# Optimization experiments

Measured on AMD Instinct MI355X. Metric: run time of the kernel, lower is better.

## Reference

```python
import jax, jax.numpy as jnp
import numpy as np

N = 500_000      # active input voxels
C = 64           # feature channels
B = 2            # batch size
RES = 256        # input spatial resolution (coords in [0, RES))
FACTOR = 2       # downsample factor (init kwarg)


def setup_inputs() -> dict:
    key = jax.random.key(0)
    k1, k2, k3 = jax.random.split(key, 3)
    feats = jax.random.normal(k1, (N, C), dtype=jnp.float32)
    bidx = jax.random.randint(k2, (N, 1), 0, B, dtype=jnp.int32)
    xyz = jax.random.randint(k3, (N, 3), 0, RES, dtype=jnp.int32)
    coords = jnp.concatenate([bidx, xyz], axis=1)  # [N, 4] = (b, x, y, z)
    return {"feats": feats, "coords": coords}


def reference(feats, coords):
    """Sparse voxel downsample: coord hashing + dedup + scatter-mean pooling.

    Returns (new_feats [N, C], new_coords [N, 4]); rows beyond the number of
    unique downsampled voxels are zero-feature / coord = -1 padding (JAX needs
    static shapes; torch original returns only the n_unique valid rows).
    """
    res = RES // FACTOR  # static spatial extent after downsampling
    b = coords[:, 0].astype(jnp.int32)
    xyz = coords[:, 1:] // FACTOR  # [N, 3]
    # linear hash code = ((b*res + x)*res + y)*res + z
    code = ((b * res + xyz[:, 0]) * res + xyz[:, 1]) * res + xyz[:, 2]
    uniq, inv = jnp.unique(code, size=N, fill_value=-1, return_inverse=True)
    # mean pooling with include_self=False == segment_sum / segment_count
    counts = jax.ops.segment_sum(jnp.ones((N,), feats.dtype), inv, num_segments=N)
    sums = jax.ops.segment_sum(feats, inv, num_segments=N)  # [N, C]
    new_feats = sums / jnp.maximum(counts, 1.0)[:, None]
    # decode unique codes back to (b, x, y, z)
    valid = counts > 0
    z = uniq % res
    y = (uniq // res) % res
    x = (uniq // (res * res)) % res
    nb = uniq // (res * res * res)
    new_coords = jnp.stack([nb, x, y, z], axis=-1).astype(jnp.int32)
    new_coords = jnp.where(valid[:, None], new_coords, -1)
    return new_feats, new_coords
```

## Files before the change

### kernel.cpp

```cpp
#include <hip/hip_runtime.h>


#define RES2 128
#define NCODES (2 * 128 * 128 * 128)
#define NW (NCODES / 4)
#define HBLK 4096

__global__ void count_codes(const int* __restrict__ coords,
                            unsigned* __restrict__ cnt8,
                            int* __restrict__ codes, int n) {
    int i = blockIdx.x * 256 + threadIdx.x;
    if (i >= n) return;
    const int4 v = reinterpret_cast<const int4*>(coords)[i];
    int code = (((v.x * RES2 + (v.y >> 1)) * RES2 + (v.z >> 1)) * RES2) + (v.w >> 1);
    codes[i] = code;
    atomicAdd(&cnt8[code >> 2], 1u << (8 * (code & 3)));
}

__global__ void block_flag_sum(const unsigned* __restrict__ cnt8,
                               unsigned* __restrict__ btot) {
    __shared__ unsigned sh[256];
    int t = threadIdx.x;
    unsigned w = cnt8[blockIdx.x * 256 + t];
    unsigned s = ((w & 0xFFu) != 0) + ((w & 0xFF00u) != 0) +
                 ((w & 0xFF0000u) != 0) + ((w & 0xFF000000u) != 0);
    sh[t] = s;
    __syncthreads();
    for (int off = 128; off > 0; off >>= 1) {
        if (t < off) sh[t] += sh[t + off];
        __syncthreads();
    }
    if (t == 0) btot[blockIdx.x] = sh[0];
}

__global__ void scan_block_totals(unsigned* __restrict__ btot,
                                  unsigned* __restrict__ nuq) {
    __shared__ unsigned sh[1024];
    int t = threadIdx.x;
    int base = t * 4;
    unsigned v[4], e[4], s = 0;
#pragma unroll
    for (int j = 0; j < 4; ++j) { v[j] = btot[base + j]; e[j] = s; s += v[j]; }
    sh[t] = s;
    __syncthreads();
    for (int off = 1; off < 1024; off <<= 1) {
        unsigned add = (t >= off) ? sh[t - off] : 0u;
        __syncthreads();
        sh[t] += add;
        __syncthreads();
    }
    unsigned excl = (t == 0) ? 0u : sh[t - 1];
#pragma unroll
    for (int j = 0; j < 4; ++j) btot[base + j] = excl + e[j];
    if (t == 1023) *nuq = sh[1023];
}

__global__ void scan_write(const unsigned* __restrict__ cnt8,
                           const unsigned* __restrict__ btot,
                           unsigned* __restrict__ rank_tab,
                           float* __restrict__ outF,
                           float* __restrict__ outC) {
    __shared__ unsigned sh[256];
    int t = threadIdx.x;
    unsigned w = cnt8[blockIdx.x * 256 + t];
    unsigned c4[4] = {w & 0xFFu, (w >> 8) & 0xFFu, (w >> 16) & 0xFFu, w >> 24};
    unsigned e[4], s = 0;
#pragma unroll
    for (int j = 0; j < 4; ++j) { e[j] = s; s += (c4[j] != 0); }
    sh[t] = s;
    __syncthreads();
    for (int off = 1; off < 256; off <<= 1) {
        unsigned add = (t >= off) ? sh[t - off] : 0u;
        __syncthreads();
        sh[t] += add;
        __syncthreads();
    }
    unsigned texcl = ((t == 0) ? 0u : sh[t - 1]) + btot[blockIdx.x];
    int cbase = (blockIdx.x * 256 + t) * 4;
#pragma unroll
    for (int j = 0; j < 4; ++j) {
        if (c4[j]) {
            unsigned r = texcl + e[j];
            int code = cbase + j;
            rank_tab[code] = r | (c4[j] << 19);
            int z = code & 127;
            int y = (code >> 7) & 127;
            int x = (code >> 14) & 127;
            int b = code >> 21;
            reinterpret_cast<float4*>(outC)[r] =
                make_float4((float)b, (float)x, (float)y, (float)z);
            if (c4[j] >= 2) {
                float4* row = reinterpret_cast<float4*>(outF + (size_t)r * 64);
                const float4 zz = make_float4(0.f, 0.f, 0.f, 0.f);
#pragma unroll
                for (int q = 0; q < 16; ++q) row[q] = zz;
            }
        }
    }
}

__global__ void tail_pad(const unsigned* __restrict__ nuq,
                         float* __restrict__ outF,
                         float* __restrict__ outC, int n) {
    int r = blockIdx.x * 256 + threadIdx.x;
    if (r >= n || r < (int)*nuq) return;
    float4* row = reinterpret_cast<float4*>(outF + (size_t)r * 64);
    const float4 zz = make_float4(0.f, 0.f, 0.f, 0.f);
#pragma unroll
    for (int q = 0; q < 16; ++q) row[q] = zz;
    reinterpret_cast<float4*>(outC)[r] = make_float4(-1.f, -1.f, -1.f, -1.f);
}

__global__ void scatter8(const float4* __restrict__ feats4,
                         const int* __restrict__ codes,
                         const unsigned* __restrict__ rank_tab,
                         float4* __restrict__ outF4, int n) {
    int tid = blockIdx.x * 256 + threadIdx.x;
    int lane = threadIdx.x & 63;
    int wave = tid >> 6;
    int q = lane >> 4;
    int sub = lane & 15;
    int ib = wave * 8;
    int i0 = ib + q;
    int i1 = ib + 4 + q;
    if (ib + 7 < n) {
        int c0 = codes[i0];
        int c1 = codes[i1];
        unsigned p0 = rank_tab[c0];
        unsigned p1 = rank_tab[c1];
        float4 v0 = feats4[(size_t)i0 * 16 + sub];
        float4 v1 = feats4[(size_t)i1 * 16 + sub];
        unsigned r0 = p0 & 0x7FFFFu, u0 = p0 >> 19;
        unsigned r1 = p1 & 0x7FFFFu, u1 = p1 >> 19;
        if (u0 == 1) {
            outF4[(size_t)r0 * 16 + sub] = v0;
        } else {
            float s = 1.0f / (float)u0;
            float* d = (float*)(outF4 + (size_t)r0 * 16 + sub);
            atomicAdd(d + 0, v0.x * s); atomicAdd(d + 1, v0.y * s);
            atomicAdd(d + 2, v0.z * s); atomicAdd(d + 3, v0.w * s);
        }
        if (u1 == 1) {
            outF4[(size_t)r1 * 16 + sub] = v1;
        } else {
            float s = 1.0f / (float)u1;
            float* d = (float*)(outF4 + (size_t)r1 * 16 + sub);
            atomicAdd(d + 0, v1.x * s); atomicAdd(d + 1, v1.y * s);
            atomicAdd(d + 2, v1.z * s); atomicAdd(d + 3, v1.w * s);
        }
    } else {
        for (int h = 0; h < 2; ++h) {
            int i = ib + h * 4 + q;
            if (i >= n) continue;
            int c = codes[i];
            unsigned p = rank_tab[c];
            unsigned r = p & 0x7FFFFu, u = p >> 19;
            float4 v = feats4[(size_t)i * 16 + sub];
            if (u == 1) {
                outF4[(size_t)r * 16 + sub] = v;
            } else {
                float s = 1.0f / (float)u;
                float* d = (float*)(outF4 + (size_t)r * 16 + sub);
                atomicAdd(d + 0, v.x * s); atomicAdd(d + 1, v.y * s);
                atomicAdd(d + 2, v.z * s); atomicAdd(d + 3, v.w * s);
            }
        }
    }
}

extern "C" void kernel_launch(void* const* d_in, const int* in_sizes, int n_in,
                              void* d_out, int out_size, void* d_ws, size_t ws_size,
                              hipStream_t stream) {
    const float* feats = (const float*)d_in[0];
    const int* coords = (const int*)d_in[1];
    const int n = in_sizes[1] / 4;

    float* outF = (float*)d_out;
    float* outC = outF + (size_t)n * 64;

    unsigned* cnt8 = (unsigned*)d_ws;
    unsigned* btot = cnt8 + NW;
    unsigned* nuq = btot + HBLK;
    int* codes = (int*)(nuq + 1);
    unsigned* rank_tab = (unsigned*)(codes + n);

    hipMemsetAsync(cnt8, 0, (size_t)NW * sizeof(unsigned), stream);

    count_codes<<<(n + 255) / 256, 256, 0, stream>>>(coords, cnt8, codes, n);
    block_flag_sum<<<HBLK, 256, 0, stream>>>(cnt8, btot);
    scan_block_totals<<<1, 1024, 0, stream>>>(btot, nuq);
    scan_write<<<HBLK, 256, 0, stream>>>(cnt8, btot, rank_tab, outF, outC);
    tail_pad<<<(n + 255) / 256, 256, 0, stream>>>(nuq, outF, outC, n);

    int waves = (n + 7) / 8;
    int blocks = (waves * 64 + 255) / 256;
    scatter8<<<blocks, 256, 0, stream>>>((const float4*)feats, codes,
                                         rank_tab, (float4*)outF, n);
}
```

Baseline: 133.7 us.

## Replace atomic scatter-mean with counting-sort bucketing and per-row gather

Extends the scan to carry both unique-count and member-count prefix sums in one 64-bit value, so each unique voxel gets a contiguous bucket. A new fill_sorted pass places input indices into these buckets with an atomic counter per row. A gather kernel then averages each bucket's features in registers and writes every output row exactly once, padding rows included. This removes the float atomics, the row pre-zeroing and the separate tail-pad kernel, at the cost of an extra index pass, extra workspace, 64-bit scans, and random feature gathers with variable per-row loop lengths.

```diff
diff --git a/kernel.cpp b/kernel.cpp
--- a/kernel.cpp
+++ b/kernel.cpp
@@ -5,6 +5,8 @@
 #define NCODES (2 * 128 * 128 * 128)
 #define NW (NCODES / 4)
 #define HBLK 4096
+
+typedef unsigned long long u64;
 
 __global__ void count_codes(const int* __restrict__ coords,
                             unsigned* __restrict__ cnt8,
@@ -17,13 +19,15 @@
     atomicAdd(&cnt8[code >> 2], 1u << (8 * (code & 3)));
 }
 
-__global__ void block_flag_sum(const unsigned* __restrict__ cnt8,
-                               unsigned* __restrict__ btot) {
-    __shared__ unsigned sh[256];
+__global__ void block_sums(const unsigned* __restrict__ cnt8,
+                           u64* __restrict__ btot) {
+    __shared__ u64 sh[256];
     int t = threadIdx.x;
     unsigned w = cnt8[blockIdx.x * 256 + t];
-    unsigned s = ((w & 0xFFu) != 0) + ((w & 0xFF00u) != 0) +
-                 ((w & 0xFF0000u) != 0) + ((w & 0xFF000000u) != 0);
+    unsigned c0 = w & 0xFFu, c1 = (w >> 8) & 0xFFu,
+             c2 = (w >> 16) & 0xFFu, c3 = w >> 24;
+    u64 s = ((u64)(c0 + c1 + c2 + c3) << 32) |
+            (u64)((c0 != 0) + (c1 != 0) + (c2 != 0) + (c3 != 0));
     sh[t] = s;
     __syncthreads();
     for (int off = 128; off > 0; off >>= 1) {
@@ -33,136 +37,163 @@
     if (t == 0) btot[blockIdx.x] = sh[0];
 }
 
-__global__ void scan_block_totals(unsigned* __restrict__ btot,
-                                  unsigned* __restrict__ nuq) {
-    __shared__ unsigned sh[1024];
+__global__ void scan_totals(u64* __restrict__ btot, unsigned* __restrict__ nuq) {
+    __shared__ u64 sh[1024];
     int t = threadIdx.x;
     int base = t * 4;
-    unsigned v[4], e[4], s = 0;
+    u64 v[4], e[4], s = 0;
 #pragma unroll
     for (int j = 0; j < 4; ++j) { v[j] = btot[base + j]; e[j] = s; s += v[j]; }
     sh[t] = s;
     __syncthreads();
     for (int off = 1; off < 1024; off <<= 1) {
-        unsigned add = (t >= off) ? sh[t - off] : 0u;
+        u64 add = (t >= off) ? sh[t - off] : 0ull;
         __syncthreads();
         sh[t] += add;
         __syncthreads();
     }
-    unsigned excl = (t == 0) ? 0u : sh[t - 1];
+    u64 excl = (t == 0) ? 0ull : sh[t - 1];
 #pragma unroll
     for (int j = 0; j < 4; ++j) btot[base + j] = excl + e[j];
-    if (t == 1023) *nuq = sh[1023];
+    if (t == 1023) *nuq = (unsigned)(sh[1023] & 0xFFFFFFFFull);
 }
 
 __global__ void scan_write(const unsigned* __restrict__ cnt8,
-                           const unsigned* __restrict__ btot,
+                           const u64* __restrict__ btot,
                            unsigned* __restrict__ rank_tab,
-                           float* __restrict__ outF,
-                           float* __restrict__ outC) {
-    __shared__ unsigned sh[256];
+                           unsigned* __restrict__ uniq_cc,
+                           unsigned* __restrict__ row_end) {
+    __shared__ u64 sh[256];
     int t = threadIdx.x;
     unsigned w = cnt8[blockIdx.x * 256 + t];
     unsigned c4[4] = {w & 0xFFu, (w >> 8) & 0xFFu, (w >> 16) & 0xFFu, w >> 24};
-    unsigned e[4], s = 0;
-#pragma unroll
-    for (int j = 0; j < 4; ++j) { e[j] = s; s += (c4[j] != 0); }
+    u64 e[4], s = 0;
+#pragma unroll
+    for (int j = 0; j < 4; ++j) {
+        e[j] = s;
+        s += ((u64)c4[j] << 32) | (u64)(c4[j] != 0);
+    }
     sh[t] = s;
     __syncthreads();
     for (int off = 1; off < 256; off <<= 1) {
-        unsigned add = (t >= off) ? sh[t - off] : 0u;
+        u64 add = (t >= off) ? sh[t - off] : 0ull;
         __syncthreads();
         sh[t] += add;
         __syncthreads();
     }
-    unsigned texcl = ((t == 0) ? 0u : sh[t - 1]) + btot[blockIdx.x];
+    u64 texcl = ((t == 0) ? 0ull : sh[t - 1]) + btot[blockIdx.x];
     int cbase = (blockIdx.x * 256 + t) * 4;
 #pragma unroll
     for (int j = 0; j < 4; ++j) {
         if (c4[j]) {
-            unsigned r = texcl + e[j];
+            unsigned r = (unsigned)((texcl + e[j]) & 0xFFFFFFFFull);
+            unsigned st = (unsigned)((texcl + e[j]) >> 32);
             int code = cbase + j;
-            rank_tab[code] = r | (c4[j] << 19);
-            int z = code & 127;
-            int y = (code >> 7) & 127;
-            int x = (code >> 14) & 127;
-            int b = code >> 21;
-            reinterpret_cast<float4*>(outC)[r] =
-                make_float4((float)b, (float)x, (float)y, (float)z);
-            if (c4[j] >= 2) {
-                float4* row = reinterpret_cast<float4*>(outF + (size_t)r * 64);
-                const float4 zz = make_float4(0.f, 0.f, 0.f, 0.f);
-#pragma unroll
-                for (int q = 0; q < 16; ++q) row[q] = zz;
-            }
-        }
-    }
-}
-
-__global__ void tail_pad(const unsigned* __restrict__ nuq,
-                         float* __restrict__ outF,
-                         float* __restrict__ outC, int n) {
-    int r = blockIdx.x * 256 + threadIdx.x;
-    if (r >= n || r < (int)*nuq) return;
-    float4* row = reinterpret_cast<float4*>(outF + (size_t)r * 64);
-    const float4 zz = make_float4(0.f, 0.f, 0.f, 0.f);
-#pragma unroll
-    for (int q = 0; q < 16; ++q) row[q] = zz;
-    reinterpret_cast<float4*>(outC)[r] = make_float4(-1.f, -1.f, -1.f, -1.f);
-}
-
-__global__ void scatter8(const float4* __restrict__ feats4,
-                         const int* __restrict__ codes,
-                         const unsigned* __restrict__ rank_tab,
-                         float4* __restrict__ outF4, int n) {
+            rank_tab[code] = r;
+            uniq_cc[r] = (unsigned)code | (c4[j] << 22);
+            row_end[r] = st;
+        }
+    }
+}
+
+__global__ void fill_sorted(const int* __restrict__ codes,
+                            const unsigned* __restrict__ rank_tab,
+                            unsigned* __restrict__ row_end,
+                            int* __restrict__ sorted_idx, int n) {
+    int i = blockIdx.x * 256 + threadIdx.x;
+    if (i >= n) return;
+    unsigned r = rank_tab[codes[i]];
+    unsigned pos = atomicAdd(&row_end[r], 1u);
+    sorted_idx[pos] = i;
+}
+
+__global__ void gather16(const float4* __restrict__ feats4,
+                         const int* __restrict__ sorted_idx,
+                         const unsigned* __restrict__ row_end,
+                         const unsigned* __restrict__ uniq_cc,
+                         const unsigned* __restrict__ nuq_p,
+                         float4* __restrict__ outF4,
+                         float4* __restrict__ outC4, int n) {
     int tid = blockIdx.x * 256 + threadIdx.x;
+    int wave = tid >> 6;
     int lane = threadIdx.x & 63;
-    int wave = tid >> 6;
     int q = lane >> 4;
     int sub = lane & 15;
-    int ib = wave * 8;
-    int i0 = ib + q;
-    int i1 = ib + 4 + q;
-    if (ib + 7 < n) {
-        int c0 = codes[i0];
-        int c1 = codes[i1];
-        unsigned p0 = rank_tab[c0];
-        unsigned p1 = rank_tab[c1];
-        float4 v0 = feats4[(size_t)i0 * 16 + sub];
-        float4 v1 = feats4[(size_t)i1 * 16 + sub];
-        unsigned r0 = p0 & 0x7FFFFu, u0 = p0 >> 19;
-        unsigned r1 = p1 & 0x7FFFFu, u1 = p1 >> 19;
-        if (u0 == 1) {
-            outF4[(size_t)r0 * 16 + sub] = v0;
-        } else {
-            float s = 1.0f / (float)u0;
-            float* d = (float*)(outF4 + (size_t)r0 * 16 + sub);
-            atomicAdd(d + 0, v0.x * s); atomicAdd(d + 1, v0.y * s);
-            atomicAdd(d + 2, v0.z * s); atomicAdd(d + 3, v0.w * s);
-        }
-        if (u1 == 1) {
-            outF4[(size_t)r1 * 16 + sub] = v1;
-        } else {
-            float s = 1.0f / (float)u1;
-            float* d = (float*)(outF4 + (size_t)r1 * 16 + sub);
-            atomicAdd(d + 0, v1.x * s); atomicAdd(d + 1, v1.y * s);
-            atomicAdd(d + 2, v1.z * s); atomicAdd(d + 3, v1.w * s);
+    int rb = wave * 16 + q;
+    int nuq = (int)*nuq_p;
+
+    int r[4];
+    bool ok[4];
+#pragma unroll
+    for (int k = 0; k < 4; ++k) { r[k] = rb + k * 4; ok[k] = (r[k] < nuq); }
+
+    bool allv = (wave * 16 + 15 < n) & ok[0] & ok[1] & ok[2] & ok[3];
+    if (allv) {
+        unsigned en[4], cc[4];
+#pragma unroll
+        for (int k = 0; k < 4; ++k) en[k] = row_end[r[k]];
+#pragma unroll
+        for (int k = 0; k < 4; ++k) cc[k] = uniq_cc[r[k]];
+        int cnt[4], st[4], i0[4];
+#pragma unroll
+        for (int k = 0; k < 4; ++k) {
+            cnt[k] = (int)(cc[k] >> 22);
+            st[k] = (int)en[k] - cnt[k];
+        }
+#pragma unroll
+        for (int k = 0; k < 4; ++k) i0[k] = sorted_idx[st[k]];
+        float4 a[4];
+#pragma unroll
+        for (int k = 0; k < 4; ++k) a[k] = feats4[(size_t)i0[k] * 16 + sub];
+#pragma unroll
+        for (int k = 0; k < 4; ++k) {
+            if (cnt[k] > 1) {
+                for (int m = 1; m < cnt[k]; ++m) {
+                    int i = sorted_idx[st[k] + m];
+                    float4 v = feats4[(size_t)i * 16 + sub];
+                    a[k].x += v.x; a[k].y += v.y; a[k].z += v.z; a[k].w += v.w;
+                }
+                float sc = 1.0f / (float)cnt[k];
+                a[k].x *= sc; a[k].y *= sc; a[k].z *= sc; a[k].w *= sc;
+            }
+            outF4[(size_t)r[k] * 16 + sub] = a[k];
+            if (sub == 0) {
+                unsigned code = cc[k] & 0x3FFFFFu;
+                outC4[r[k]] = make_float4((float)(code >> 21),
+                                          (float)((code >> 14) & 127),
+                                          (float)((code >> 7) & 127),
+                                          (float)(code & 127));
+            }
         }
     } else {
-        for (int h = 0; h < 2; ++h) {
-            int i = ib + h * 4 + q;
-            if (i >= n) continue;
-            int c = codes[i];
-            unsigned p = rank_tab[c];
-            unsigned r = p & 0x7FFFFu, u = p >> 19;
-            float4 v = feats4[(size_t)i * 16 + sub];
-            if (u == 1) {
-                outF4[(size_t)r * 16 + sub] = v;
+#pragma unroll
+        for (int k = 0; k < 4; ++k) {
+            if (r[k] >= n) continue;
+            if (ok[k]) {
+                unsigned en = row_end[r[k]];
+                unsigned cc = uniq_cc[r[k]];
+                int cnt = (int)(cc >> 22);
+                int st = (int)en - cnt;
+                float4 a = make_float4(0.f, 0.f, 0.f, 0.f);
+                for (int m = 0; m < cnt; ++m) {
+                    int i = sorted_idx[st + m];
+                    float4 v = feats4[(size_t)i * 16 + sub];
+                    a.x += v.x; a.y += v.y; a.z += v.z; a.w += v.w;
+                }
+                float sc = 1.0f / (float)cnt;
+                a.x *= sc; a.y *= sc; a.z *= sc; a.w *= sc;
+                outF4[(size_t)r[k] * 16 + sub] = a;
+                if (sub == 0) {
+                    unsigned code = cc & 0x3FFFFFu;
+                    outC4[r[k]] = make_float4((float)(code >> 21),
+                                              (float)((code >> 14) & 127),
+                                              (float)((code >> 7) & 127),
+                                              (float)(code & 127));
+                }
             } else {
-                float s = 1.0f / (float)u;
-                float* d = (float*)(outF4 + (size_t)r * 16 + sub);
-                atomicAdd(d + 0, v.x * s); atomicAdd(d + 1, v.y * s);
-                atomicAdd(d + 2, v.z * s); atomicAdd(d + 3, v.w * s);
+                outF4[(size_t)r[k] * 16 + sub] = make_float4(0.f, 0.f, 0.f, 0.f);
+                if (sub == 0)
+                    outC4[r[k]] = make_float4(-1.f, -1.f, -1.f, -1.f);
             }
         }
     }
@@ -176,24 +207,28 @@
     const int n = in_sizes[1] / 4;
 
     float* outF = (float*)d_out;
-    float* outC = outF + (size_t)n * 64;
+    float4* outC4 = (float4*)(outF + (size_t)n * 64);
 
     unsigned* cnt8 = (unsigned*)d_ws;
-    unsigned* btot = cnt8 + NW;
-    unsigned* nuq = btot + HBLK;
-    int* codes = (int*)(nuq + 1);
+    u64* btot = (u64*)(cnt8 + NW);
+    unsigned* nuq = (unsigned*)(btot + HBLK);
+    int* codes = (int*)(nuq + 2);
     unsigned* rank_tab = (unsigned*)(codes + n);
+    unsigned* uniq_cc = rank_tab + NCODES;
+    unsigned* row_end = uniq_cc + n;
+    int* sorted_idx = (int*)(row_end + n);
 
     hipMemsetAsync(cnt8, 0, (size_t)NW * sizeof(unsigned), stream);
 
     count_codes<<<(n + 255) / 256, 256, 0, stream>>>(coords, cnt8, codes, n);
-    block_flag_sum<<<HBLK, 256, 0, stream>>>(cnt8, btot);
-    scan_block_totals<<<1, 1024, 0, stream>>>(btot, nuq);
-    scan_write<<<HBLK, 256, 0, stream>>>(cnt8, btot, rank_tab, outF, outC);
-    tail_pad<<<(n + 255) / 256, 256, 0, stream>>>(nuq, outF, outC, n);
-
-    int waves = (n + 7) / 8;
+    block_sums<<<HBLK, 256, 0, stream>>>(cnt8, btot);
+    scan_totals<<<1, 1024, 0, stream>>>(btot, nuq);
+    scan_write<<<HBLK, 256, 0, stream>>>(cnt8, btot, rank_tab, uniq_cc, row_end);
+    fill_sorted<<<(n + 255) / 256, 256, 0, stream>>>(codes, rank_tab, row_end, sorted_idx, n);
+
+    int waves = (n + 15) / 16;
     int blocks = (waves * 64 + 255) / 256;
-    scatter8<<<blocks, 256, 0, stream>>>((const float4*)feats, codes,
-                                         rank_tab, (float4*)outF, n);
-}
+    gather16<<<blocks, 256, 0, stream>>>((const float4*)feats, sorted_idx,
+                                         row_end, uniq_cc, nuq,
+                                         (float4*)outF, outC4, n);
+}
```

Result: faster. 125.6 us (-6.0%).

## Replace per-code rank table with per-word prefix and recompute rank in scatter

Applied to the files above, without the earlier changes.

scan_write now stores one exclusive prefix per packed count word instead of scattering a rank/count entry into a code-indexed table. scatter8 reads the count word and word prefix and recomputes the rank and multiplicity from the byte flags. This swaps scattered rank-table writes for a dense, coalesced prefix array. Singleton rows are now written with nontemporal stores. The cost is one extra dependent gather per point in scatter.

```diff
diff --git a/kernel.cpp b/kernel.cpp
--- a/kernel.cpp
+++ b/kernel.cpp
@@ -5,6 +5,8 @@
 #define NCODES (2 * 128 * 128 * 128)
 #define NW (NCODES / 4)
 #define HBLK 4096
+
+typedef float f4 __attribute__((ext_vector_type(4)));
 
 __global__ void count_codes(const int* __restrict__ coords,
                             unsigned* __restrict__ cnt8,
@@ -22,9 +24,8 @@
     __shared__ unsigned sh[256];
     int t = threadIdx.x;
     unsigned w = cnt8[blockIdx.x * 256 + t];
-    unsigned s = ((w & 0xFFu) != 0) + ((w & 0xFF00u) != 0) +
-                 ((w & 0xFF0000u) != 0) + ((w & 0xFF000000u) != 0);
-    sh[t] = s;
+    sh[t] = ((w & 0xFFu) != 0) + (((w >> 8) & 0xFFu) != 0) +
+            (((w >> 16) & 0xFFu) != 0) + ((w >> 24) != 0);
     __syncthreads();
     for (int off = 128; off > 0; off >>= 1) {
         if (t < off) sh[t] += sh[t + off];
@@ -33,8 +34,8 @@
     if (t == 0) btot[blockIdx.x] = sh[0];
 }
 
-__global__ void scan_block_totals(unsigned* __restrict__ btot,
-                                  unsigned* __restrict__ nuq) {
+__global__ void scan_totals(unsigned* __restrict__ btot,
+                            unsigned* __restrict__ nuq) {
     __shared__ unsigned sh[1024];
     int t = threadIdx.x;
     int base = t * 4;
@@ -57,12 +58,13 @@
 
 __global__ void scan_write(const unsigned* __restrict__ cnt8,
                            const unsigned* __restrict__ btot,
-                           unsigned* __restrict__ rank_tab,
-                           float* __restrict__ outF,
-                           float* __restrict__ outC) {
+                           unsigned* __restrict__ wprefix,
+                           f4* __restrict__ outF4,
+                           f4* __restrict__ outC4) {
     __shared__ unsigned sh[256];
     int t = threadIdx.x;
-    unsigned w = cnt8[blockIdx.x * 256 + t];
+    int widx = blockIdx.x * 256 + t;
+    unsigned w = cnt8[widx];
     unsigned c4[4] = {w & 0xFFu, (w >> 8) & 0xFFu, (w >> 16) & 0xFFu, w >> 24};
     unsigned e[4], s = 0;
 #pragma unroll
@@ -76,22 +78,19 @@
         __syncthreads();
     }
     unsigned texcl = ((t == 0) ? 0u : sh[t - 1]) + btot[blockIdx.x];
-    int cbase = (blockIdx.x * 256 + t) * 4;
+    wprefix[widx] = texcl;
+    int cbase = widx * 4;
 #pragma unroll
     for (int j = 0; j < 4; ++j) {
         if (c4[j]) {
             unsigned r = texcl + e[j];
             int code = cbase + j;
-            rank_tab[code] = r | (c4[j] << 19);
-            int z = code & 127;
-            int y = (code >> 7) & 127;
-            int x = (code >> 14) & 127;
-            int b = code >> 21;
-            reinterpret_cast<float4*>(outC)[r] =
-                make_float4((float)b, (float)x, (float)y, (float)z);
+            f4 cv = {(float)(code >> 21), (float)((code >> 14) & 127),
+                     (float)((code >> 7) & 127), (float)(code & 127)};
+            outC4[r] = cv;
             if (c4[j] >= 2) {
-                float4* row = reinterpret_cast<float4*>(outF + (size_t)r * 64);
-                const float4 zz = make_float4(0.f, 0.f, 0.f, 0.f);
+                f4* row = outF4 + (size_t)r * 16;
+                const f4 zz = {0.f, 0.f, 0.f, 0.f};
 #pragma unroll
                 for (int q = 0; q < 16; ++q) row[q] = zz;
             }
@@ -100,70 +99,55 @@
 }
 
 __global__ void tail_pad(const unsigned* __restrict__ nuq,
-                         float* __restrict__ outF,
-                         float* __restrict__ outC, int n) {
+                         f4* __restrict__ outF4,
+                         f4* __restrict__ outC4, int n) {
     int r = blockIdx.x * 256 + threadIdx.x;
     if (r >= n || r < (int)*nuq) return;
-    float4* row = reinterpret_cast<float4*>(outF + (size_t)r * 64);
-    const float4 zz = make_float4(0.f, 0.f, 0.f, 0.f);
+    f4* row = outF4 + (size_t)r * 16;
+    const f4 zz = {0.f, 0.f, 0.f, 0.f};
 #pragma unroll
     for (int q = 0; q < 16; ++q) row[q] = zz;
-    reinterpret_cast<float4*>(outC)[r] = make_float4(-1.f, -1.f, -1.f, -1.f);
+    f4 mm = {-1.f, -1.f, -1.f, -1.f};
+    outC4[r] = mm;
 }
 
-__global__ void scatter8(const float4* __restrict__ feats4,
+__global__ void scatter8(const f4* __restrict__ feats4,
                          const int* __restrict__ codes,
-                         const unsigned* __restrict__ rank_tab,
-                         float4* __restrict__ outF4, int n) {
+                         const unsigned* __restrict__ cnt8,
+                         const unsigned* __restrict__ wprefix,
+                         f4* __restrict__ outF4, int n) {
     int tid = blockIdx.x * 256 + threadIdx.x;
     int lane = threadIdx.x & 63;
     int wave = tid >> 6;
     int q = lane >> 4;
     int sub = lane & 15;
     int ib = wave * 8;
-    int i0 = ib + q;
-    int i1 = ib + 4 + q;
-    if (ib + 7 < n) {
-        int c0 = codes[i0];
-        int c1 = codes[i1];
-        unsigned p0 = rank_tab[c0];
-        unsigned p1 = rank_tab[c1];
-        float4 v0 = feats4[(size_t)i0 * 16 + sub];
-        float4 v1 = feats4[(size_t)i1 * 16 + sub];
-        unsigned r0 = p0 & 0x7FFFFu, u0 = p0 >> 19;
-        unsigned r1 = p1 & 0x7FFFFu, u1 = p1 >> 19;
-        if (u0 == 1) {
-            outF4[(size_t)r0 * 16 + sub] = v0;
+
+#pragma unroll
+    for (int h = 0; h < 2; ++h) {
+        int i = ib + h * 4 + q;
+        if (i >= n) continue;
+        int c = codes[i];
+        unsigned w = cnt8[c >> 2];
+        unsigned base = wprefix[c >> 2];
+        int j = c & 3;
+        unsigned cnt = (w >> (8 * j)) & 0xFFu;
+        unsigned occ = 0;
+        if (j > 0) occ += ((w & 0xFFu) != 0);
+        if (j > 1) occ += (((w >> 8) & 0xFFu) != 0);
+        if (j > 2) occ += (((w >> 16) & 0xFFu) != 0);
+        unsigned r = base + occ;
+        f4 v = feats4[(size_t)i * 16 + sub];
+        f4* dst = outF4 + (size_t)r * 16 + sub;
+        if (cnt == 1) {
+            __builtin_nontemporal_store(v, dst);
         } else {
-            float s = 1.0f / (float)u0;
-            float* d = (float*)(outF4 + (size_t)r0 * 16 + sub);
-            atomicAdd(d + 0, v0.x * s); atomicAdd(d + 1, v0.y * s);
-            atomicAdd(d + 2, v0.z * s); atomicAdd(d + 3, v0.w * s);
-        }
-        if (u1 == 1) {
-            outF4[(size_t)r1 * 16 + sub] = v1;
-        } else {
-            float s = 1.0f / (float)u1;
-            float* d = (float*)(outF4 + (size_t)r1 * 16 + sub);
-            atomicAdd(d + 0, v1.x * s); atomicAdd(d + 1, v1.y * s);
-            atomicAdd(d + 2, v1.z * s); atomicAdd(d + 3, v1.w * s);
-        }
-    } else {
-        for (int h = 0; h < 2; ++h) {
-            int i = ib + h * 4 + q;
-            if (i >= n) continue;
-            int c = codes[i];
-            unsigned p = rank_tab[c];
-            unsigned r = p & 0x7FFFFu, u = p >> 19;
-            float4 v = feats4[(size_t)i * 16 + sub];
-            if (u == 1) {
-                outF4[(size_t)r * 16 + sub] = v;
-            } else {
-                float s = 1.0f / (float)u;
-                float* d = (float*)(outF4 + (size_t)r * 16 + sub);
-                atomicAdd(d + 0, v.x * s); atomicAdd(d + 1, v.y * s);
-                atomicAdd(d + 2, v.z * s); atomicAdd(d + 3, v.w * s);
-            }
+            float sc = 1.0f / (float)cnt;
+            float* d = (float*)dst;
+            atomicAdd(d + 0, v.x * sc);
+            atomicAdd(d + 1, v.y * sc);
+            atomicAdd(d + 2, v.z * sc);
+            atomicAdd(d + 3, v.w * sc);
         }
     }
 }
@@ -176,24 +160,25 @@
     const int n = in_sizes[1] / 4;
 
     float* outF = (float*)d_out;
-    float* outC = outF + (size_t)n * 64;
+    f4* outF4 = (f4*)outF;
+    f4* outC4 = (f4*)(outF + (size_t)n * 64);
 
     unsigned* cnt8 = (unsigned*)d_ws;
     unsigned* btot = cnt8 + NW;
     unsigned* nuq = btot + HBLK;
     int* codes = (int*)(nuq + 1);
-    unsigned* rank_tab = (unsigned*)(codes + n);
+    unsigned* wprefix = (unsigned*)(codes + n);
 
-    hipMemsetAsync(cnt8, 0, (size_t)NW * sizeof(unsigned), stream);
+    (void)hipMemsetAsync(cnt8, 0, (size_t)NW * sizeof(unsigned), stream);
 
     count_codes<<<(n + 255) / 256, 256, 0, stream>>>(coords, cnt8, codes, n);
     block_flag_sum<<<HBLK, 256, 0, stream>>>(cnt8, btot);
-    scan_block_totals<<<1, 1024, 0, stream>>>(btot, nuq);
-    scan_write<<<HBLK, 256, 0, stream>>>(cnt8, btot, rank_tab, outF, outC);
-    tail_pad<<<(n + 255) / 256, 256, 0, stream>>>(nuq, outF, outC, n);
+    scan_totals<<<1, 1024, 0, stream>>>(btot, nuq);
+    scan_write<<<HBLK, 256, 0, stream>>>(cnt8, btot, wprefix, outF4, outC4);
+    tail_pad<<<(n + 255) / 256, 256, 0, stream>>>(nuq, outF4, outC4, n);
 
     int waves = (n + 7) / 8;
     int blocks = (waves * 64 + 255) / 256;
-    scatter8<<<blocks, 256, 0, stream>>>((const float4*)feats, codes,
-                                         rank_tab, (float4*)outF, n);
+    scatter8<<<blocks, 256, 0, stream>>>((const f4*)feats, codes, cnt8,
+                                         wprefix, outF4, n);
 }
```

Result: no change. 133.3 us (-0.3%).
